# Optimization experiments

Hardware: AMD Instinct MI355X
Metric: run time of the kernel (lower is better)

## Reference

```python
import jax, jax.numpy as jnp
import numpy as np
from jax import lax

GAMMA = 1.0
BIG = 1e10  # finite 'infinity' to keep softmin gradients well-defined
EPS = 1e-8


def _cosine_cost(x, y):
    # x: [B,M,D], y: [B,N,D] -> cost [B,M,N] = 1 - cos_sim
    xn = x / (jnp.linalg.norm(x, axis=-1, keepdims=True) + EPS)
    yn = y / (jnp.linalg.norm(y, axis=-1, keepdims=True) + EPS)
    return 1.0 - jnp.einsum('bmd,bnd->bmn', xn, yn)


def _softdtw_from_cost(D, gamma=GAMMA):
    # Anti-diagonal soft-DTW DP. D: [B,M,N] -> [B]
    B, M, N = D.shape
    ii = jnp.arange(M + 1)
    prev = jnp.full((B, M + 1), BIG, D.dtype).at[:, 0].set(0.0)  # diag k=0
    prev2 = jnp.full((B, M + 1), BIG, D.dtype)                   # diag k=-1

    def shift(a):  # a[i] -> a[i-1], pad with BIG
        return jnp.concatenate([jnp.full((B, 1), BIG, a.dtype), a[:, :-1]], axis=1)

    def step(carry, k):
        p2, p1 = carry
        jj = k - ii
        valid = (ii >= 1) & (jj >= 1) & (ii <= M) & (jj <= N)
        di = jnp.clip(ii - 1, 0, M - 1)
        dj = jnp.clip(jj - 1, 0, N - 1)
        d = D[:, di, dj]                      # [B, M+1] cost along diagonal
        a = shift(p1)                          # R[i-1, j]
        b = p1                                 # R[i, j-1]
        c = shift(p2)                          # R[i-1, j-1]
        smin = -gamma * jax.nn.logsumexp(jnp.stack([-a, -b, -c]) / gamma, axis=0)
        new = jnp.where(valid[None, :], d + smin, BIG)
        return (p1, new), None

    (_, last), _ = lax.scan(step, (prev2, prev), jnp.arange(1, M + N + 1))
    return last[:, M]  # R[M, N]


def _sdtw(x, y):
    # SoftDTW(gamma=1, normalize=True, dist='cosine')
    raw_xy = _softdtw_from_cost(_cosine_cost(x, y))
    raw_xx = _softdtw_from_cost(_cosine_cost(x, x))
    raw_yy = _softdtw_from_cost(_cosine_cost(y, y))
    return raw_xy - 0.5 * (raw_xx + raw_yy)


def setup_inputs() -> dict:
    key = jax.random.key(0)
    k1, k2, k3, k4 = jax.random.split(key, 4)
    B, T, D = 32, 512, 128
    return {
        'TGT': jax.random.normal(k1, (B, T, D), jnp.float32),
        'OTH': jax.random.normal(k2, (B, T, D), jnp.float32),
        'X': jax.random.normal(k3, (B, T, D), jnp.float32),
        'labels': jax.random.normal(k4, (B,), jnp.float32),
    }


def reference(TGT, OTH, X, labels):
    diff = _sdtw(OTH, X) - _sdtw(TGT, X)   # [B]
    return jnp.mean((diff - labels) ** 2)  # MSELoss
```

## Files before the change

kernel.cpp:

```cpp
#include <hip/hip_runtime.h>
#include <hip/hip_bf16.h>

#define LOG2E 1.4426950408889634f
#define LN2   0.6931471805599453f

#define BATCH 32
#define SEQ   512
#define DIM   128
#define NMAT  128

#define EXP2F(x) __builtin_amdgcn_exp2f(x)
#define LOG2F(x) __builtin_amdgcn_logf(x)

typedef short bf16x8 __attribute__((ext_vector_type(8)));
typedef float f32x4 __attribute__((ext_vector_type(4)));
typedef __attribute__((address_space(1))) const void gas_void;
typedef __attribute__((address_space(3))) void las_void;

__device__ __forceinline__ float dpp_shr1(float x) {
  return __int_as_float(__builtin_amdgcn_update_dpp(
      0, __float_as_int(x), 0x138, 0xF, 0xF, false));
}
__device__ __forceinline__ float dpp_shl1(float x) {
  return __int_as_float(__builtin_amdgcn_update_dpp(
      0, __float_as_int(x), 0x130, 0xF, 0xF, false));
}
template <int CTRL>
__device__ __forceinline__ float dpp_max(float x) {
  int y = __builtin_amdgcn_update_dpp(
      __float_as_int(x), __float_as_int(x), CTRL, 0xF, 0xF, false);
  return fmaxf(x, __int_as_float(y));
}

__device__ __forceinline__ unsigned short f2bf_rn(float f) {
  unsigned u = __float_as_uint(f);
  u = (u + 0x7FFF + ((u >> 16) & 1)) >> 16;
  return (unsigned short)u;
}
__device__ __forceinline__ float bf2f(unsigned short h) {
  return __uint_as_float(((unsigned)h) << 16);
}

__global__ __launch_bounds__(256) void prep_kernel(
    const float* __restrict__ tgt, const float* __restrict__ oth,
    const float* __restrict__ x, unsigned short* __restrict__ Y) {
  int gid  = blockIdx.x * blockDim.x + threadIdx.x;
  int wave = gid >> 6;
  int lane = threadIdx.x & 63;
  int set = wave / (BATCH * SEQ);
  int row = wave % (BATCH * SEQ);
  const float* src = (set == 0) ? tgt : ((set == 1) ? oth : x);
  const float2* p = (const float2*)(src + (size_t)row * DIM);
  float2 v = p[lane];
  float s = v.x * v.x + v.y * v.y;
#pragma unroll
  for (int off = 32; off; off >>= 1) s += __shfl_xor(s, off);
  float inv = 1.0f / (sqrtf(s) + 1e-8f);
  float y0 = v.x * inv, y1 = v.y * inv;
  unsigned short h0 = f2bf_rn(y0);
  unsigned short l0 = f2bf_rn(y0 - bf2f(h0));
  unsigned short h1 = f2bf_rn(y1);
  unsigned short l1 = f2bf_rn(y1 - bf2f(h1));
  ushort4 st = {h0, l0, h1, l1};
  ((ushort4*)(Y + (size_t)wave * 256))[lane] = st;
}

__global__ __launch_bounds__(256) void costmm_kernel(
    const unsigned short* __restrict__ Y, float* __restrict__ Sband) {
  __shared__ unsigned short As[64 * 64];
  __shared__ unsigned short Bs[192 * 64];

  const int m = blockIdx.x;
  const int s = blockIdx.y;
  const int p = m >> 5, b = m & 31;
  const int setA = (p == 1 || p == 3) ? 0 : 1;
  const int setB = (p <= 1) ? 2 : setA;
  const unsigned short* YA = Y + ((size_t)(setA * BATCH + b)) * SEQ * 256;
  const unsigned short* YB = Y + ((size_t)(setB * BATCH + b)) * SEQ * 256;
  const int i0 = s * 64;
  const int j0 = s * 64 - 64;

  const int t = threadIdx.x;
  const int w = t >> 6, l = t & 63;

  f32x4 acc[4][3];
#pragma unroll
  for (int a = 0; a < 4; ++a)
#pragma unroll
    for (int c = 0; c < 3; ++c) acc[a][c] = (f32x4){0.f, 0.f, 0.f, 0.f};

  const int srow_off = l >> 3;
  const int scb      = ((l & 7) * 16) ^ ((srow_off & 7) * 16);

  for (int slab = 0; slab < 4; ++slab) {
    if (slab) __syncthreads();
#pragma unroll
    for (int q2 = 0; q2 < 2; ++q2) {
      int wi = w * 2 + q2;
      int r = wi * 8 + srow_off;
      const unsigned short* gA = YA + (size_t)(i0 + r) * 256 + slab * 64 + (scb >> 1);
      __builtin_amdgcn_global_load_lds((gas_void*)gA, (las_void*)(As + wi * 512), 16, 0, 0);
    }
#pragma unroll
    for (int q6 = 0; q6 < 6; ++q6) {
      int wi = w * 6 + q6;
      int r = wi * 8 + srow_off;
      int j = j0 + r; j = (j < 0) ? 0 : ((j > 511) ? 511 : j);
      const unsigned short* gB = YB + (size_t)j * 256 + slab * 64 + (scb >> 1);
      __builtin_amdgcn_global_load_lds((gas_void*)gB, (las_void*)(Bs + wi * 512), 16, 0, 0);
    }
    asm volatile("s_waitcnt vmcnt(0)" ::: "memory");
    __syncthreads();

#pragma unroll
    for (int ks = 0; ks < 2; ++ks) {
      bf16x8 af[4], bfr[3];
#pragma unroll
      for (int f = 0; f < 4; ++f) {
        int ra = f * 16 + (l & 15);
        int ca = (ks * 64 + (l >> 4) * 16) ^ ((ra & 7) << 4);
        af[f] = *(const bf16x8*)((const char*)As + ra * 128 + ca);
      }
#pragma unroll
      for (int f = 0; f < 3; ++f) {
        int rb = w * 48 + f * 16 + (l & 15);
        int cb = (ks * 64 + (l >> 4) * 16) ^ ((rb & 7) << 4);
        bfr[f] = *(const bf16x8*)((const char*)Bs + rb * 128 + cb);
      }
#pragma unroll
      for (int fm = 0; fm < 4; ++fm)
#pragma unroll
        for (int fn = 0; fn < 3; ++fn)
          acc[fm][fn] = __builtin_amdgcn_mfma_f32_16x16x32_bf16(
              af[fm], bfr[fn], acc[fm][fn], 0, 0, 0);
    }
  }

  float* Sbm = Sband + (size_t)m * (SEQ * 128);
#pragma unroll
  for (int fm = 0; fm < 4; ++fm)
#pragma unroll
    for (int fn = 0; fn < 3; ++fn)
#pragma unroll
      for (int q = 0; q < 4; ++q) {
        int r = fm * 16 + (l >> 4) * 4 + q;
        int c = w * 48 + fn * 16 + (l & 15);
        unsigned crm = (unsigned)(c - r);
        if (crm < 128u) {
          int jreal = j0 + c;
          float dp = (1.0f - acc[fm][fn][q]) * LOG2E;
          float sval = ((unsigned)jreal < 512u) ? EXP2F(-dp) : 0.0f;
          Sbm[((size_t)(i0 + r) << 7) + crm] = sval;
        }
      }
}

__global__ __launch_bounds__(64) void dtw_kernel(
    const float* __restrict__ Sband, const float* __restrict__ zerorow,
    float* __restrict__ raw) {
  __shared__ float stg[128][128];
  const int t = threadIdx.x;
  const int m = blockIdx.x;
  const float* Db = Sband + (size_t)m * (SEQ * 128);

  float v0 = (t == 32) ? 1.0f : 0.0f;
  float v1 = 0.0f;
  int otally = 0;

  {
    float4 z4 = make_float4(0.f, 0.f, 0.f, 0.f);
#pragma unroll
    for (int q = 0; q < 32; ++q) {
      int row = 64 + q * 2 + (t >> 5);
      *(float4*)&stg[row][(t & 31) * 4] = z4;
    }
  }
#pragma unroll
  for (int q = 0; q < 32; ++q) {
    int row = q * 2;
    __builtin_amdgcn_global_load_lds(
        (gas_void*)(Db + (size_t)row * 128 + t * 4),
        (las_void*)(&stg[row][0]), 16, 0, 0);
  }

#define CHUNK(C_)                                                             \
  {                                                                           \
    const int c = (C_);                                                       \
    {                                                                         \
      int rbase = 16 * c + 64;                                                \
      _Pragma("unroll")                                                       \
      for (int q = 0; q < 8; ++q) {                                           \
        int row = rbase + q * 2;                                              \
        int srow = row + (t >> 5);                                            \
        const float* src = (srow < 512) ? (Db + (size_t)srow * 128 + (t & 31) * 4) \
                                        : (zerorow + (t & 31) * 4);           \
        __builtin_amdgcn_global_load_lds((gas_void*)src,                      \
            (las_void*)(&stg[row & 127][0]), 16, 0, 0);                       \
      }                                                                       \
    }                                                                         \
    asm volatile("s_waitcnt vmcnt(8)" ::: "memory");                          \
    float sv[32];                                                             \
    const int Lb = 32 * c + 1;                                                \
    const int ra = 16 * c + 31 - t;                                           \
    sv[0] = stg[ra & 127][2 * t + 1];                                         \
    _Pragma("unroll")                                                         \
    for (int k = 1; k <= 15; ++k) {                                           \
      float2 xy = *(const float2*)&stg[(ra + k) & 127][2 * t];                \
      sv[2 * k - 1] = xy.x;                                                   \
      sv[2 * k]     = xy.y;                                                   \
    }                                                                         \
    sv[31] = stg[(ra + 16) & 127][2 * t];                                     \
    _Pragma("unroll")                                                         \
    for (int qq = 0; qq < 32; qq += 2) {                                      \
      {                                                                       \
        float a = dpp_shl1(v0);                                               \
        v1 = sv[qq] * (a + v0 + v1);                                          \
      }                                                                       \
      {                                                                       \
        float bb = dpp_shr1(v1);                                              \
        v0 = sv[qq + 1] * (v1 + bb + v0);                                     \
      }                                                                       \
    }                                                                         \
    (void)Lb;                                                                 \
  }

  for (int cc = 0; cc < 16; ++cc) {
    CHUNK(2 * cc)
    CHUNK(2 * cc + 1)
    float mx = fmaxf(v0, v1);
    mx = dpp_max<0x111>(mx);
    mx = dpp_max<0x112>(mx);
    mx = dpp_max<0x114>(mx);
    mx = dpp_max<0x118>(mx);
    mx = dpp_max<0x142>(mx);
    mx = dpp_max<0x143>(mx);
    float mxs = __int_as_float(
        __builtin_amdgcn_readlane(__float_as_int(mx), 63));
    int e = (int)((__float_as_uint(mxs) >> 23) & 255u) - 127;
    float scale = __uint_as_float((unsigned)(127 - e) << 23);
    v0 *= scale; v1 *= scale;
    otally += e;
  }
#undef CHUNK

  if (t == 32) raw[m] = -(LOG2F(v0) + (float)otally) * LN2;
}

__global__ __launch_bounds__(64) void combine_kernel(
    const float* __restrict__ raw, const float* __restrict__ labels,
    float* __restrict__ out) {
  int lane = threadIdx.x;
  float val = 0.0f;
  if (lane < BATCH) {
    float r0 = raw[0 * BATCH + lane];
    float r1 = raw[1 * BATCH + lane];
    float r2 = raw[2 * BATCH + lane];
    float r3 = raw[3 * BATCH + lane];
    float diff = r0 - r1 - 0.5f * r2 + 0.5f * r3;
    float e = diff - labels[lane];
    val = e * e;
  }
#pragma unroll
  for (int off = 32; off; off >>= 1) val += __shfl_xor(val, off);
  if (lane == 0) out[0] = val * (1.0f / BATCH);
}

extern "C" void kernel_launch(void* const* d_in, const int* in_sizes, int n_in,
                              void* d_out, int out_size, void* d_ws, size_t ws_size,
                              hipStream_t stream) {
  const float* TGT = (const float*)d_in[0];
  const float* OTH = (const float*)d_in[1];
  const float* X   = (const float*)d_in[2];
  const float* labels = (const float*)d_in[3];
  float* out = (float*)d_out;

  char* ws = (char*)d_ws;
  float* Sband = (float*)ws;
  size_t sband_bytes = (size_t)NMAT * SEQ * 128 * 4;
  unsigned short* Y = (unsigned short*)(ws + sband_bytes);
  size_t y_bytes = (size_t)3 * BATCH * SEQ * 256 * 2;
  float* raw = (float*)(ws + sband_bytes + y_bytes);
  float* zerorow = raw + NMAT;

  hipMemsetAsync(zerorow, 0, 512, stream);
  hipLaunchKernelGGL(prep_kernel, dim3((3 * BATCH * SEQ) / 4), dim3(256), 0, stream,
                     TGT, OTH, X, Y);
  hipLaunchKernelGGL(costmm_kernel, dim3(NMAT, 8), dim3(256), 0, stream, Y, Sband);
  hipLaunchKernelGGL(dtw_kernel, dim3(NMAT), dim3(64), 0, stream, Sband, zerorow, raw);
  hipLaunchKernelGGL(combine_kernel, dim3(1), dim3(64), 0, stream, raw, labels, out);
}
```

Baseline: 70.88 us.

## Run DTW recursion bidirectionally from both ends and meet in the middle

The banded soft-DTW recursion now runs a forward pass from the start and a backward pass from the end at the same time in one wave, each covering half the diagonals. The two halves are joined at the middle by a cross-lane reduction. The goal is to halve the length of the serial dependency chain and interleave two independent chains to hide DPP and FMA latency. It costs double the LDS staging buffers, extra register pressure and a more complex join step. The costmm grid is also swapped to (8, NMAT) so that neighbouring blocks work on the same matrix.

```diff
diff --git a/kernel.cpp b/kernel.cpp
--- a/kernel.cpp
+++ b/kernel.cpp
@@ -70,8 +70,8 @@
   __shared__ unsigned short As[64 * 64];
   __shared__ unsigned short Bs[192 * 64];
 
-  const int m = blockIdx.x;
-  const int s = blockIdx.y;
+  const int s = blockIdx.x;
+  const int m = blockIdx.y;
   const int p = m >> 5, b = m & 31;
   const int setA = (p == 1 || p == 3) ? 0 : 1;
   const int setB = (p <= 1) ? 2 : setA;
@@ -158,21 +158,22 @@
 __global__ __launch_bounds__(64) void dtw_kernel(
     const float* __restrict__ Sband, const float* __restrict__ zerorow,
     float* __restrict__ raw) {
-  __shared__ float stg[128][128];
+  __shared__ float stf[128][128];
+  __shared__ float stb[128][128];
   const int t = threadIdx.x;
   const int m = blockIdx.x;
   const float* Db = Sband + (size_t)m * (SEQ * 128);
 
-  float v0 = (t == 32) ? 1.0f : 0.0f;
-  float v1 = 0.0f;
-  int otally = 0;
+  float v0  = (t == 32) ? 1.0f : 0.0f, v1  = 0.0f;
+  float v0b = (t == 32) ? 1.0f : 0.0f, v1b = 0.0f;
+  int otf = 0, otb = 0;
 
   {
     float4 z4 = make_float4(0.f, 0.f, 0.f, 0.f);
 #pragma unroll
-    for (int q = 0; q < 32; ++q) {
-      int row = 64 + q * 2 + (t >> 5);
-      *(float4*)&stg[row][(t & 31) * 4] = z4;
+    for (int q = 0; q < 16; ++q) {
+      int row = 96 + q * 2 + (t >> 5);
+      *(float4*)&stf[row][(t & 31) * 4] = z4;
     }
   }
 #pragma unroll
@@ -180,70 +181,108 @@
     int row = q * 2;
     __builtin_amdgcn_global_load_lds(
         (gas_void*)(Db + (size_t)row * 128 + t * 4),
-        (las_void*)(&stg[row][0]), 16, 0, 0);
-  }
-
-#define CHUNK(C_)                                                             \
+        (las_void*)(&stf[row][0]), 16, 0, 0);
+  }
+#pragma unroll
+  for (int q = 0; q < 40; ++q) {
+    int row = 464 + q * 2;
+    int srow = row + (t >> 5);
+    const float* src = (srow < 512) ? (Db + (size_t)srow * 128 + (t & 31) * 4)
+                                    : (zerorow + (t & 31) * 4);
+    __builtin_amdgcn_global_load_lds((gas_void*)src,
+        (las_void*)(&stb[row & 127][0]), 16, 0, 0);
+  }
+
+#define CHUNKFB(C_)                                                           \
   {                                                                           \
     const int c = (C_);                                                       \
-    {                                                                         \
+    {               \
       int rbase = 16 * c + 64;                                                \
       _Pragma("unroll")                                                       \
       for (int q = 0; q < 8; ++q) {                                           \
         int row = rbase + q * 2;                                              \
         int srow = row + (t >> 5);                                            \
-        const float* src = (srow < 512) ? (Db + (size_t)srow * 128 + (t & 31) * 4) \
-                                        : (zerorow + (t & 31) * 4);           \
-        __builtin_amdgcn_global_load_lds((gas_void*)src,                      \
-            (las_void*)(&stg[row & 127][0]), 16, 0, 0);                       \
+        __builtin_amdgcn_global_load_lds(                                     \
+            (gas_void*)(Db + (size_t)srow * 128 + (t & 31) * 4),              \
+            (las_void*)(&stf[row & 127][0]), 16, 0, 0);                       \
       }                                                                       \
     }                                                                         \
-    asm volatile("s_waitcnt vmcnt(8)" ::: "memory");                          \
-    float sv[32];                                                             \
-    const int Lb = 32 * c + 1;                                                \
-    const int ra = 16 * c + 31 - t;                                           \
-    sv[0] = stg[ra & 127][2 * t + 1];                                         \
+    {            \
+      int rbase = 448 - 16 * c;                                               \
+      _Pragma("unroll")                                                       \
+      for (int q = 0; q < 8; ++q) {                                           \
+        int row = rbase + q * 2;                                              \
+        int srow = row + (t >> 5);                                            \
+        __builtin_amdgcn_global_load_lds(                                     \
+            (gas_void*)(Db + (size_t)srow * 128 + (t & 31) * 4),              \
+            (las_void*)(&stb[row & 127][0]), 16, 0, 0);                       \
+      }                                                                       \
+    }                                                                         \
+    asm volatile("s_waitcnt vmcnt(16)" ::: "memory");                        \
+    float svf[32], svb[32];                                                   \
+    const int raf = 16 * c + 31 - t;                                          \
+    svf[0] = stf[raf & 127][2 * t + 1];                                       \
     _Pragma("unroll")                                                         \
     for (int k = 1; k <= 15; ++k) {                                           \
-      float2 xy = *(const float2*)&stg[(ra + k) & 127][2 * t];                \
-      sv[2 * k - 1] = xy.x;                                                   \
-      sv[2 * k]     = xy.y;                                                   \
-    }                                                                         \
-    sv[31] = stg[(ra + 16) & 127][2 * t];                                     \
+      float2 xy = *(const float2*)&stf[(raf + k) & 127][2 * t];               \
+      svf[2 * k - 1] = xy.x;                                                  \
+      svf[2 * k]     = xy.y;                                                  \
+    }                                                                         \
+    svf[31] = stf[(raf + 16) & 127][2 * t];                                   \
+    const int rab = 512 - 16 * c + 31 - t;                                    \
+    svb[0] = stb[rab & 127][2 * t];                                           \
+    _Pragma("unroll")                                                         \
+    for (int k = 1; k <= 15; ++k) {                                           \
+      float2 xy = *(const float2*)&stb[(rab - k) & 127][2 * t];               \
+      svb[2 * k - 1] = xy.y;                                                  \
+      svb[2 * k]     = xy.x;                                                  \
+    }                                                                         \
+    svb[31] = stb[(rab - 16) & 127][2 * t + 1];                               \
     _Pragma("unroll")                                                         \
     for (int qq = 0; qq < 32; qq += 2) {                                      \
-      {                                                                       \
-        float a = dpp_shl1(v0);                                               \
-        v1 = sv[qq] * (a + v0 + v1);                                          \
-      }                                                                       \
-      {                                                                       \
-        float bb = dpp_shr1(v1);                                              \
-        v0 = sv[qq + 1] * (v1 + bb + v0);                                     \
-      }                                                                       \
-    }                                                                         \
-    (void)Lb;                                                                 \
-  }
-
-  for (int cc = 0; cc < 16; ++cc) {
-    CHUNK(2 * cc)
-    CHUNK(2 * cc + 1)
-    float mx = fmaxf(v0, v1);
-    mx = dpp_max<0x111>(mx);
-    mx = dpp_max<0x112>(mx);
-    mx = dpp_max<0x114>(mx);
-    mx = dpp_max<0x118>(mx);
-    mx = dpp_max<0x142>(mx);
-    mx = dpp_max<0x143>(mx);
-    float mxs = __int_as_float(
-        __builtin_amdgcn_readlane(__float_as_int(mx), 63));
-    int e = (int)((__float_as_uint(mxs) >> 23) & 255u) - 127;
-    float scale = __uint_as_float((unsigned)(127 - e) << 23);
-    v0 *= scale; v1 *= scale;
-    otally += e;
-  }
-#undef CHUNK
-
-  if (t == 32) raw[m] = -(LOG2F(v0) + (float)otally) * LN2;
+                                                    \
+      float af = dpp_shl1(v0);                                                \
+      v1 = svf[qq] * ((v0 + v1) + af);                                        \
+                                                              \
+      float ab = dpp_shr1(v1b);                                               \
+      v0b = svb[qq] * ((v1b + v0b) + ab);                                     \
+                                                              \
+      float bf = dpp_shr1(v1);                                                \
+      v0 = svf[qq + 1] * ((v1 + v0) + bf);                                    \
+                                                               \
+      float bb = dpp_shl1(v0b);                                               \
+      v1b = svb[qq + 1] * ((v0b + v1b) + bb);                                 \
+    }                                                                         \
+  }
+
+  for (int cc = 0; cc < 8; ++cc) {
+    CHUNKFB(2 * cc)
+    CHUNKFB(2 * cc + 1)
+    float mf = fmaxf(v0, v1);
+    mf = dpp_max<0x111>(mf); mf = dpp_max<0x112>(mf);
+    mf = dpp_max<0x114>(mf); mf = dpp_max<0x118>(mf);
+    mf = dpp_max<0x142>(mf); mf = dpp_max<0x143>(mf);
+    float mfs = __int_as_float(__builtin_amdgcn_readlane(__float_as_int(mf), 63));
+    int ef = (int)((__float_as_uint(mfs) >> 23) & 255u) - 127;
+    float sf = __uint_as_float((unsigned)(127 - ef) << 23);
+    v0 *= sf; v1 *= sf; otf += ef;
+
+    float mb = fmaxf(v0b, v1b);
+    mb = dpp_max<0x111>(mb); mb = dpp_max<0x112>(mb);
+    mb = dpp_max<0x114>(mb); mb = dpp_max<0x118>(mb);
+    mb = dpp_max<0x142>(mb); mb = dpp_max<0x143>(mb);
+    float mbs = __int_as_float(__builtin_amdgcn_readlane(__float_as_int(mb), 63));
+    int eb = (int)((__float_as_uint(mbs) >> 23) & 255u) - 127;
+    float sb = __uint_as_float((unsigned)(127 - eb) << 23);
+    v0b *= sb; v1b *= sb; otb += eb;
+  }
+#undef CHUNKFB
+
+  float shb = dpp_shr1(v1b);
+  float term = v0 * ((v1b + shb) + v0b) + v1 * v1b;
+#pragma unroll
+  for (int off = 32; off; off >>= 1) term += __shfl_xor(term, off);
+  if (t == 32) raw[m] = -(LOG2F(term) + (float)(otf + otb)) * LN2;
 }
 
 __global__ __launch_bounds__(64) void combine_kernel(
@@ -285,7 +324,7 @@
   hipMemsetAsync(zerorow, 0, 512, stream);
   hipLaunchKernelGGL(prep_kernel, dim3((3 * BATCH * SEQ) / 4), dim3(256), 0, stream,
                      TGT, OTH, X, Y);
-  hipLaunchKernelGGL(costmm_kernel, dim3(NMAT, 8), dim3(256), 0, stream, Y, Sband);
+  hipLaunchKernelGGL(costmm_kernel, dim3(8, NMAT), dim3(256), 0, stream, Y, Sband);
   hipLaunchKernelGGL(dtw_kernel, dim3(NMAT), dim3(64), 0, stream, Sband, zerorow, raw);
   hipLaunchKernelGGL(combine_kernel, dim3(1), dim3(64), 0, stream, raw, labels, out);
 }
```

Result: faster. 63.44 us (-10.5%).
